# Performance work log

Measured on AMD Instinct MI355X. Metric: run time of the kernel, lower is better.

## Reference

```python
import jax, jax.numpy as jnp
import numpy as np

B, T, D, H = 2, 2048, 1024, 16
HD = D // H  # head_dim = 64


def setup_inputs() -> dict:
    key = jax.random.key(0)
    ks = jax.random.split(key, 6)
    x = jax.random.normal(ks[0], (B, T, D), dtype=jnp.float32)
    wq = jax.random.normal(ks[1], (D, D), dtype=jnp.float32) * (D ** -0.5)
    wk = jax.random.normal(ks[2], (D, D), dtype=jnp.float32) * (D ** -0.5)
    wv = jax.random.normal(ks[3], (D, D), dtype=jnp.float32) * (D ** -0.5)
    wo = jax.random.normal(ks[4], (D, D), dtype=jnp.float32) * (D ** -0.5)
    # RoPE tables: standard inverse-frequency angles, shape [T, head_dim]
    inv_freq = 1.0 / (10000.0 ** (jnp.arange(0, HD, 2, dtype=jnp.float32) / HD))
    ang = jnp.arange(T, dtype=jnp.float32)[:, None] * inv_freq[None, :]  # [T, HD/2]
    ang = jnp.concatenate([ang, ang], axis=-1)  # [T, HD]
    cos, sin = jnp.cos(ang), jnp.sin(ang)
    # causal mask [1,1,T,T]: True where attention is allowed
    mask = jnp.tril(jnp.ones((T, T), dtype=bool))[None, None]
    return {"x": x, "wq": wq, "wk": wk, "wv": wv, "wo": wo,
            "cos": cos, "sin": sin, "mask": mask}


def rotate_half(u):
    u1, u2 = jnp.split(u, 2, axis=-1)
    return jnp.concatenate([-u2, u1], axis=-1)


def reference(x, wq, wk, wv, wo, cos, sin, mask):
    b, t, c = x.shape
    # projections (nn.Linear: y = x @ W^T), reshape to [B, H, T, HD]
    def proj(w):
        return (x @ w.T).reshape(b, t, H, HD).transpose(0, 2, 1, 3)
    q, k, v = proj(wq), proj(wk), proj(wv)
    # inline RoPE: cos/sin broadcast [1,1,T,HD]
    co = cos[:t][None, None]
    si = sin[:t][None, None]
    q = q * co + rotate_half(q) * si
    k = k * co + rotate_half(k) * si
    # scaled dot-product attention with causal mask
    att = jnp.einsum("bhqd,bhkd->bhqk", q, k) * (HD ** -0.5)
    att = jnp.where(mask[:, :, :t, :t], att, -jnp.inf)
    att = jax.nn.softmax(att, axis=-1)
    out = jnp.einsum("bhqk,bhkd->bhqd", att, v)
    out = out.transpose(0, 2, 1, 3).reshape(b, t, c)
    return out @ wo.T
```

## Files before the change

### kernel.cpp

```cpp
#include <hip/hip_runtime.h>
#include <hip/hip_bf16.h>
#include <type_traits>

#define B_  2
#define T_  2048
#define D_  1024
#define H_  16
#define HD_ 64

typedef __attribute__((ext_vector_type(8))) short bf16x8;
typedef __attribute__((ext_vector_type(4))) float f32x4;

__device__ __forceinline__ unsigned short f2b(float x) {
  union { __hip_bfloat16 h; unsigned short u; } c;
  c.h = __float2bfloat16(x);
  return c.u;
}
__device__ __forceinline__ float b2f(unsigned short u) {
  union { unsigned short u; __hip_bfloat16 h; } c;
  c.u = u;
  return __bfloat162float(c.h);
}

__device__ __forceinline__ void ld_g2l_16(const unsigned short* g, unsigned short* l) {
  auto gp = (const __attribute__((address_space(1))) unsigned int*)g;
  auto lp = (__attribute__((address_space(3))) unsigned int*)l;
  __builtin_amdgcn_global_load_lds(gp, lp, 16, 0, 0);
}

__global__ void __launch_bounds__(256)
cast_all(const float* __restrict__ x, const float* __restrict__ wq,
         const float* __restrict__ wk, const float* __restrict__ wv,
         const float* __restrict__ wo, unsigned short* __restrict__ xb,
         unsigned short* __restrict__ wp) {
  int blk = blockIdx.x;
  const float* src;
  unsigned short* dst;
  size_t off;
  if (blk < 2048) {
    src = x; dst = xb; off = (size_t)blk * 2048;
  } else {
    int t = (blk - 2048) >> 9;
    int r = (blk - 2048) & 511;
    src = (t == 0) ? wq : (t == 1) ? wk : (t == 2) ? wv : wo;
    dst = wp + (size_t)t * 1048576;
    off = (size_t)r * 2048;
  }
  size_t i = off + threadIdx.x * 8;
  float4 a = *(const float4*)(src + i);
  float4 b = *(const float4*)(src + i + 4);
  unsigned short h[8] = {f2b(a.x), f2b(a.y), f2b(a.z), f2b(a.w),
                         f2b(b.x), f2b(b.y), f2b(b.z), f2b(b.w)};
  *(uint4*)(dst + i) = *(uint4*)h;
}

template <typename OutT, int MROWS>
__device__ __forceinline__ void gemm_core(const unsigned short* __restrict__ A,
                                          const unsigned short* __restrict__ Bw,
                                          OutT* __restrict__ C, int K, int Ldc,
                                          int rope_mode, const float* __restrict__ cosT,
                                          const float* __restrict__ sinT, int tok0) {
  constexpr int MT = MROWS / 32;
  constexpr int ASZ = MROWS * 32;
  __shared__ __align__(16) unsigned short shm[2 * ASZ + 2 * 128 * 32];
  const int tid = threadIdx.x;
  const int lane = tid & 63;
  const int w = tid >> 6;
  const int m16 = lane & 15;
  const int quad = lane >> 4;
  const int wm = w >> 1, wn = w & 1;
  const int rl = lane >> 2;
  const int cl = (lane & 3) * 8;

  auto a_sp = [&](int bs) { return &shm[bs * ASZ]; };
  auto b_sp = [&](int bs) { return &shm[2 * ASZ + bs * 4096]; };

  f32x4 acc[MT][4];
#pragma unroll
  for (int i = 0; i < MT; i++)
#pragma unroll
    for (int j = 0; j < 4; j++) acc[i][j] = (f32x4){0.f, 0.f, 0.f, 0.f};

  auto stage = [&](int it, int bs) {
    int k0 = it * 32;
#pragma unroll
    for (int t = 0; t < MROWS / 64; t++) {
      int seg = w * 16 + t * 64;
      ld_g2l_16(A + (size_t)(seg + rl) * K + k0 + cl, a_sp(bs) + seg * 32);
    }
#pragma unroll
    for (int j2 = 0; j2 < 2; j2++) {
      int seg = w * 32 + j2 * 16;
      ld_g2l_16(Bw + (size_t)(seg + rl) * K + k0 + cl, b_sp(bs) + seg * 32);
    }
  };

  const int nit = K / 32;
  stage(0, 0);
  __syncthreads();
  for (int it = 0; it < nit; it++) {
    int cur = it & 1;
    if (it + 1 < nit) stage(it + 1, cur ^ 1);
    bf16x8 af[MT], bfr[4];
#pragma unroll
    for (int mt = 0; mt < MT; mt++)
      af[mt] = *(const bf16x8*)(a_sp(cur) + (wm * (MT * 16) + mt * 16 + m16) * 32 + quad * 8);
#pragma unroll
    for (int nt = 0; nt < 4; nt++)
      bfr[nt] = *(const bf16x8*)(b_sp(cur) + (wn * 64 + nt * 16 + m16) * 32 + quad * 8);
#pragma unroll
    for (int mt = 0; mt < MT; mt++)
#pragma unroll
      for (int nt = 0; nt < 4; nt++)
        acc[mt][nt] = __builtin_amdgcn_mfma_f32_16x16x32_bf16(af[mt], bfr[nt], acc[mt][nt], 0, 0, 0);
    __syncthreads();
  }

  if (rope_mode == 3) {
    if constexpr (std::is_same_v<OutT, unsigned short> && MROWS == 128) {
#pragma unroll
      for (int p = 0; p < 2; p++) {
        if (wn == p) {
#pragma unroll
          for (int mt = 0; mt < MT; mt++)
#pragma unroll
            for (int nt = 0; nt < 4; nt++) {
              int r = nt * 16 + m16;
              int s = wm * 16 + mt * 4 + quad;
              unsigned short pk[4] = {f2b(acc[mt][nt][0]), f2b(acc[mt][nt][1]),
                                      f2b(acc[mt][nt][2]), f2b(acc[mt][nt][3])};
              *(uint2*)&shm[r * 136 + s * 4] = *(uint2*)pk;
            }
        }
        __syncthreads();
#pragma unroll
        for (int i = 0; i < 8; i++) {
          int li = i * 256 + tid;
          int r = li >> 5, s = li & 31;
          *(uint2*)(C + (size_t)(p * 64 + r) * T_ + s * 4) =
              *(const uint2*)&shm[r * 136 + s * 4];
        }
        __syncthreads();
      }
    }
    return;
  }

  if (rope_mode == 1 || rope_mode == 2) {
    float scale = (rope_mode == 2) ? 0.18033688011112042f : 1.f;
#pragma unroll
    for (int mt = 0; mt < MT; mt++)
#pragma unroll
      for (int reg = 0; reg < 4; reg++) {
        int t = (tok0 + wm * (MT * 16) + mt * 16 + quad * 4 + reg) & (T_ - 1);
#pragma unroll
        for (int nt = 0; nt < 2; nt++) {
          int d = nt * 16 + m16;
          float co = cosT[t * HD_ + d] * scale;
          float si = sinT[t * HD_ + d] * scale;
          float lo = acc[mt][nt][reg], hi = acc[mt][nt + 2][reg];
          acc[mt][nt][reg]     = lo * co - hi * si;
          acc[mt][nt + 2][reg] = hi * co + lo * si;
        }
      }
  }
#pragma unroll
  for (int mt = 0; mt < MT; mt++)
#pragma unroll
    for (int nt = 0; nt < 4; nt++)
#pragma unroll
      for (int reg = 0; reg < 4; reg++) {
        OutT* p = C + (size_t)(wm * (MT * 16) + mt * 16 + quad * 4 + reg) * Ldc + wn * 64 + nt * 16 + m16;
        if constexpr (std::is_same_v<OutT, float>) *p = acc[mt][nt][reg];
        else *p = f2b(acc[mt][nt][reg]);
      }
}

__global__ void __launch_bounds__(256)
gemm_qkv(const unsigned short* __restrict__ xb, const unsigned short* __restrict__ wp,
         unsigned short* __restrict__ qkv, const float* __restrict__ cosT,
         const float* __restrict__ sinT) {
  const int nb = blockIdx.x;
  const int bm = blockIdx.y * 128;
  const int mi = nb >> 3;
  const int bn = (nb & 7) * 128;
  if (mi == 2) {
    unsigned short* Cv = qkv + 2 * (4096ull * D_) +
                         (size_t)(bm >> 11) * (size_t)(H_ * HD_) * T_ +
                         (size_t)bn * T_ + (bm & (T_ - 1));
    gemm_core<unsigned short, 128>(xb + (size_t)bm * D_,
                                   wp + (size_t)(2 * 1024 + bn) * D_,
                                   Cv, D_, T_, 3, nullptr, nullptr, bm);
  } else {
    const int rope_mode = (mi == 0) ? 2 : 1;
    gemm_core<unsigned short, 128>(xb + (size_t)bm * D_,
                                   wp + (size_t)(mi * 1024 + bn) * D_,
                                   qkv + (size_t)mi * (4096ull * D_) + (size_t)bm * D_ + bn,
                                   D_, D_, rope_mode, cosT, sinT, bm);
  }
}

__global__ void __launch_bounds__(256)
gemm_out(const unsigned short* __restrict__ Ab, const unsigned short* __restrict__ wob,
         float* __restrict__ C) {
  const int bn = blockIdx.x * 128;
  const int bm = blockIdx.y * 64;
  gemm_core<float, 64>(Ab + (size_t)bm * D_, wob + (size_t)bn * D_,
                       C + (size_t)bm * D_ + bn, D_, D_, 0, nullptr, nullptr, 0);
}

__global__ void __launch_bounds__(256, 3)
attn_kernel(const unsigned short* __restrict__ Q, const unsigned short* __restrict__ K,
            const unsigned short* __restrict__ VT, unsigned short* __restrict__ O) {
  __shared__ __align__(16) unsigned short qp_s[64][72];
  __shared__ __align__(16) unsigned short k_s[2][64 * 64];
  __shared__ __align__(16) unsigned short vt_s[2][64 * 64];

  const int tid = threadIdx.x;
  const int lane = tid & 63;
  const int w = tid >> 6;
  const int m16 = lane & 15;
  const int quad = lane >> 4;
  const int swz = m16 & 7;
  const int pc0 = quad ^ swz;
  const int pc1 = pc0 ^ 4;

  const int x = blockIdx.x;
  const int qt = 31 - (x >> 5);
  const int bh = x & 31;
  const int b = bh >> 4, h = bh & 15;
  const int q0 = qt * 64;

  const unsigned short* Qb = Q + ((size_t)b * T_ + q0) * D_ + h * HD_;
  const unsigned short* Kb = K + (size_t)b * T_ * D_ + h * HD_;
  const unsigned short* VTb = VT + ((size_t)b * H_ + h) * HD_ * T_;

#pragma unroll
  for (int i = 0; i < 2; i++) {
    int idx = tid + i * 256;
    int r = idx >> 3, c = idx & 7;
    *(bf16x8*)&qp_s[r][c * 8] = *(const bf16x8*)(Qb + (size_t)r * D_ + c * 8);
  }

  auto stage_kv = [&](int kt, int bs) {
    int rs = lane >> 3;
    int cs = ((lane & 7) ^ rs) * 8;
    int gr = w * 16 + rs;
    ld_g2l_16(Kb + (size_t)(kt * 64 + gr) * D_ + cs,      &k_s[bs][(w * 16) * 64]);
    ld_g2l_16(Kb + (size_t)(kt * 64 + gr + 8) * D_ + cs,  &k_s[bs][(w * 16 + 8) * 64]);
    ld_g2l_16(VTb + (size_t)gr * T_ + kt * 64 + cs,       &vt_s[bs][(w * 16) * 64]);
    ld_g2l_16(VTb + (size_t)(gr + 8) * T_ + kt * 64 + cs, &vt_s[bs][(w * 16 + 8) * 64]);
  };

  f32x4 o_acc[4];
#pragma unroll
  for (int dt = 0; dt < 4; dt++) o_acc[dt] = (f32x4){0.f, 0.f, 0.f, 0.f};
  float m_i = -1e30f, l_i = 0.f;
  const int rg = q0 + w * 16 + m16;

  stage_kv(0, 0);
  __syncthreads();
  bf16x8 q_frag[2];
  q_frag[0] = *(const bf16x8*)&qp_s[w * 16 + m16][quad * 8];
  q_frag[1] = *(const bf16x8*)&qp_s[w * 16 + m16][32 + quad * 8];

  for (int t = 0; t <= qt; t++) {
    int cur = t & 1;
    if (t < qt) stage_kv(t + 1, cur ^ 1);

    const unsigned short* kc = &k_s[cur][0];
    const unsigned short* vc = &vt_s[cur][0];
    f32x4 sf[4];
    __builtin_amdgcn_s_setprio(1);
#pragma unroll
    for (int jt = 0; jt < 4; jt++) {
      bf16x8 a0 = *(const bf16x8*)&kc[(jt * 16 + m16) * 64 + pc0 * 8];
      bf16x8 a1 = *(const bf16x8*)&kc[(jt * 16 + m16) * 64 + pc1 * 8];
      f32x4 acc = (f32x4){0.f, 0.f, 0.f, 0.f};
      acc = __builtin_amdgcn_mfma_f32_16x16x32_bf16(a0, q_frag[0], acc, 0, 0, 0);
      acc = __builtin_amdgcn_mfma_f32_16x16x32_bf16(a1, q_frag[1], acc, 0, 0, 0);
      sf[jt] = acc;
    }
    __builtin_amdgcn_s_setprio(0);
    if (t == qt) {
#pragma unroll
      for (int jt = 0; jt < 4; jt++)
#pragma unroll
        for (int reg = 0; reg < 4; reg++) {
          int jg = t * 64 + jt * 16 + quad * 4 + reg;
          if (jg > rg) sf[jt][reg] = -1e30f;
        }
    }
    float mx = sf[0][0];
#pragma unroll
    for (int jt = 0; jt < 4; jt++)
#pragma unroll
      for (int reg = 0; reg < 4; reg++) mx = fmaxf(mx, sf[jt][reg]);
    mx = fmaxf(mx, __shfl_xor(mx, 16, 64));
    mx = fmaxf(mx, __shfl_xor(mx, 32, 64));
    if (!__all(mx <= m_i + 8.f)) {
      float mn = fmaxf(m_i, mx);
      float alpha = exp2f(m_i - mn);
      l_i *= alpha;
#pragma unroll
      for (int dt = 0; dt < 4; dt++)
#pragma unroll
        for (int reg = 0; reg < 4; reg++) o_acc[dt][reg] *= alpha;
      m_i = mn;
    }
    float lt = 0.f;
    float p[4][4];
#pragma unroll
    for (int jt = 0; jt < 4; jt++)
#pragma unroll
      for (int reg = 0; reg < 4; reg++) {
        p[jt][reg] = exp2f(sf[jt][reg] - m_i);
        lt += p[jt][reg];
      }
#pragma unroll
    for (int jt = 0; jt < 4; jt++) {
      unsigned short pk[4] = {f2b(p[jt][0]), f2b(p[jt][1]), f2b(p[jt][2]), f2b(p[jt][3])};
      *(uint2*)&qp_s[w * 16 + m16][jt * 16 + quad * 4] = *(uint2*)pk;
    }
    bf16x8 bp0 = *(const bf16x8*)&qp_s[w * 16 + m16][quad * 8];
    bf16x8 bp1 = *(const bf16x8*)&qp_s[w * 16 + m16][32 + quad * 8];
    __builtin_amdgcn_s_setprio(1);
#pragma unroll
    for (int dt = 0; dt < 4; dt++) {
      int rowd = dt * 16 + m16;
      bf16x8 a0 = *(const bf16x8*)&vc[rowd * 64 + pc0 * 8];
      bf16x8 a1 = *(const bf16x8*)&vc[rowd * 64 + pc1 * 8];
      o_acc[dt] = __builtin_amdgcn_mfma_f32_16x16x32_bf16(a0, bp0, o_acc[dt], 0, 0, 0);
      o_acc[dt] = __builtin_amdgcn_mfma_f32_16x16x32_bf16(a1, bp1, o_acc[dt], 0, 0, 0);
    }
    __builtin_amdgcn_s_setprio(0);
    lt += __shfl_xor(lt, 16, 64);
    lt += __shfl_xor(lt, 32, 64);
    l_i += lt;
    __syncthreads();
  }

  float inv = 1.f / l_i;
#pragma unroll
  for (int dt = 0; dt < 4; dt++) {
    unsigned short ok[4];
#pragma unroll
    for (int reg = 0; reg < 4; reg++) ok[reg] = f2b(o_acc[dt][reg] * inv);
    *(uint2*)&qp_s[w * 16 + m16][dt * 16 + quad * 4] = *(uint2*)ok;
  }
  __syncthreads();
  unsigned short* Ob = O + ((size_t)b * T_ + q0) * D_ + h * HD_;
#pragma unroll
  for (int i = 0; i < 2; i++) {
    int idx = tid + i * 256;
    int r = idx >> 3, c = idx & 7;
    *(bf16x8*)(Ob + (size_t)r * D_ + c * 8) = *(const bf16x8*)&qp_s[r][c * 8];
  }
}

extern "C" void kernel_launch(void* const* d_in, const int* in_sizes, int n_in,
                              void* d_out, int out_size, void* d_ws, size_t ws_size,
                              hipStream_t stream) {
  const float* x    = (const float*)d_in[0];
  const float* wq   = (const float*)d_in[1];
  const float* wk   = (const float*)d_in[2];
  const float* wv   = (const float*)d_in[3];
  const float* wo   = (const float*)d_in[4];
  const float* cosT = (const float*)d_in[5];
  const float* sinT = (const float*)d_in[6];
  float* out = (float*)d_out;

  const size_t NTOK = (size_t)B_ * T_;
  const size_t SZ   = NTOK * D_;
  unsigned short* xb   = (unsigned short*)d_ws;
  unsigned short* Wp   = xb + SZ;
  unsigned short* QKVh = Wp + 4 * 1048576;
  unsigned short* Ab   = QKVh + 3 * SZ;

  cast_all<<<4096, 256, 0, stream>>>(x, wq, wk, wv, wo, xb, Wp);
  gemm_qkv<<<dim3(24, 32), 256, 0, stream>>>(xb, Wp, QKVh, cosT, sinT);
  attn_kernel<<<1024, 256, 0, stream>>>(QKVh, QKVh + SZ, QKVh + 2 * SZ, Ab);
  gemm_out<<<dim3(8, 64), 256, 0, stream>>>(Ab, Wp + 3 * 1048576, out);
}
```

Measured before the change: 203.5 us.

## Fuse all four stages into one persistent cooperative kernel with grid syncs

Replaces the four separate launches (cast, QKV GEMM, attention, output GEMM) with a single cooperative kernel of 768 blocks that runs each stage in turn, separated by grid-wide barriers. The four launch gaps and tail idle time are meant to go away. Attention work is redistributed so blocks 0-255 take two q-tiles, paired as x and 1023-x, and the rest take one, to balance the causal workload. Shared memory is a single pool sized for the largest stage. Risks are the cost of grid.sync, occupancy limited to 3 blocks per CU, and the output GEMM using only 512 of the blocks. It falls back to the old four launches if the cooperative launch fails.

Result: slower. 651.3 us (+220.1%).

```diff
diff --git a/kernel.cpp b/kernel.cpp
--- a/kernel.cpp
+++ b/kernel.cpp
@@ -1,12 +1,16 @@
 #include <hip/hip_runtime.h>
 #include <hip/hip_bf16.h>
+#include <hip/hip_cooperative_groups.h>
 #include <type_traits>
+
+namespace cg = cooperative_groups;
 
 #define B_  2
 #define T_  2048
 #define D_  1024
 #define H_  16
 #define HD_ 64
+#define NB_ 768
 
 typedef __attribute__((ext_vector_type(8))) short bf16x8;
 typedef __attribute__((ext_vector_type(4))) float f32x4;
@@ -16,11 +20,6 @@
   c.h = __float2bfloat16(x);
   return c.u;
 }
-__device__ __forceinline__ float b2f(unsigned short u) {
-  union { unsigned short u; __hip_bfloat16 h; } c;
-  c.u = u;
-  return __bfloat162float(c.h);
-}
 
 __device__ __forceinline__ void ld_g2l_16(const unsigned short* g, unsigned short* l) {
   auto gp = (const __attribute__((address_space(1))) unsigned int*)g;
@@ -28,12 +27,11 @@
   __builtin_amdgcn_global_load_lds(gp, lp, 16, 0, 0);
 }
 
-__global__ void __launch_bounds__(256)
-cast_all(const float* __restrict__ x, const float* __restrict__ wq,
-         const float* __restrict__ wk, const float* __restrict__ wv,
-         const float* __restrict__ wo, unsigned short* __restrict__ xb,
-         unsigned short* __restrict__ wp) {
-  int blk = blockIdx.x;
+__device__ __forceinline__ void cast_job(int blk, const float* __restrict__ x,
+                                         const float* __restrict__ wq, const float* __restrict__ wk,
+                                         const float* __restrict__ wv, const float* __restrict__ wo,
+                                         unsigned short* __restrict__ xb,
+                                         unsigned short* __restrict__ wp) {
   const float* src;
   unsigned short* dst;
   size_t off;
@@ -55,14 +53,14 @@
 }
 
 template <typename OutT, int MROWS>
-__device__ __forceinline__ void gemm_core(const unsigned short* __restrict__ A,
+__device__ __forceinline__ void gemm_core(unsigned short* __restrict__ shm,
+                                          const unsigned short* __restrict__ A,
                                           const unsigned short* __restrict__ Bw,
                                           OutT* __restrict__ C, int K, int Ldc,
                                           int rope_mode, const float* __restrict__ cosT,
                                           const float* __restrict__ sinT, int tok0) {
   constexpr int MT = MROWS / 32;
   constexpr int ASZ = MROWS * 32;
-  __shared__ __align__(16) unsigned short shm[2 * ASZ + 2 * 128 * 32];
   const int tid = threadIdx.x;
   const int lane = tid & 63;
   const int w = tid >> 6;
@@ -72,9 +70,6 @@
   const int rl = lane >> 2;
   const int cl = (lane & 3) * 8;
 
-  auto a_sp = [&](int bs) { return &shm[bs * ASZ]; };
-  auto b_sp = [&](int bs) { return &shm[2 * ASZ + bs * 4096]; };
-
   f32x4 acc[MT][4];
 #pragma unroll
   for (int i = 0; i < MT; i++)
@@ -86,12 +81,12 @@
 #pragma unroll
     for (int t = 0; t < MROWS / 64; t++) {
       int seg = w * 16 + t * 64;
-      ld_g2l_16(A + (size_t)(seg + rl) * K + k0 + cl, a_sp(bs) + seg * 32);
+      ld_g2l_16(A + (size_t)(seg + rl) * K + k0 + cl, shm + bs * ASZ + seg * 32);
     }
 #pragma unroll
     for (int j2 = 0; j2 < 2; j2++) {
       int seg = w * 32 + j2 * 16;
-      ld_g2l_16(Bw + (size_t)(seg + rl) * K + k0 + cl, b_sp(bs) + seg * 32);
+      ld_g2l_16(Bw + (size_t)(seg + rl) * K + k0 + cl, shm + 2 * ASZ + bs * 4096 + seg * 32);
     }
   };
 
@@ -104,10 +99,10 @@
     bf16x8 af[MT], bfr[4];
 #pragma unroll
     for (int mt = 0; mt < MT; mt++)
-      af[mt] = *(const bf16x8*)(a_sp(cur) + (wm * (MT * 16) + mt * 16 + m16) * 32 + quad * 8);
+      af[mt] = *(const bf16x8*)(shm + cur * ASZ + (wm * (MT * 16) + mt * 16 + m16) * 32 + quad * 8);
 #pragma unroll
     for (int nt = 0; nt < 4; nt++)
-      bfr[nt] = *(const bf16x8*)(b_sp(cur) + (wn * 64 + nt * 16 + m16) * 32 + quad * 8);
+      bfr[nt] = *(const bf16x8*)(shm + 2 * ASZ + cur * 4096 + (wn * 64 + nt * 16 + m16) * 32 + quad * 8);
 #pragma unroll
     for (int mt = 0; mt < MT; mt++)
 #pragma unroll
@@ -176,45 +171,38 @@
       }
 }
 
-__global__ void __launch_bounds__(256)
-gemm_qkv(const unsigned short* __restrict__ xb, const unsigned short* __restrict__ wp,
-         unsigned short* __restrict__ qkv, const float* __restrict__ cosT,
-         const float* __restrict__ sinT) {
-  const int nb = blockIdx.x;
-  const int bm = blockIdx.y * 128;
+__device__ __forceinline__ void qkv_job(unsigned short* shm, int nb, int bm,
+                                        const unsigned short* __restrict__ xb,
+                                        const unsigned short* __restrict__ wp,
+                                        unsigned short* __restrict__ qkv,
+                                        const float* __restrict__ cosT,
+                                        const float* __restrict__ sinT) {
   const int mi = nb >> 3;
   const int bn = (nb & 7) * 128;
   if (mi == 2) {
     unsigned short* Cv = qkv + 2 * (4096ull * D_) +
                          (size_t)(bm >> 11) * (size_t)(H_ * HD_) * T_ +
                          (size_t)bn * T_ + (bm & (T_ - 1));
-    gemm_core<unsigned short, 128>(xb + (size_t)bm * D_,
+    gemm_core<unsigned short, 128>(shm, xb + (size_t)bm * D_,
                                    wp + (size_t)(2 * 1024 + bn) * D_,
                                    Cv, D_, T_, 3, nullptr, nullptr, bm);
   } else {
     const int rope_mode = (mi == 0) ? 2 : 1;
-    gemm_core<unsigned short, 128>(xb + (size_t)bm * D_,
+    gemm_core<unsigned short, 128>(shm, xb + (size_t)bm * D_,
                                    wp + (size_t)(mi * 1024 + bn) * D_,
                                    qkv + (size_t)mi * (4096ull * D_) + (size_t)bm * D_ + bn,
                                    D_, D_, rope_mode, cosT, sinT, bm);
   }
 }
 
-__global__ void __launch_bounds__(256)
-gemm_out(const unsigned short* __restrict__ Ab, const unsigned short* __restrict__ wob,
-         float* __restrict__ C) {
-  const int bn = blockIdx.x * 128;
-  const int bm = blockIdx.y * 64;
-  gemm_core<float, 64>(Ab + (size_t)bm * D_, wob + (size_t)bn * D_,
-                       C + (size_t)bm * D_ + bn, D_, D_, 0, nullptr, nullptr, 0);
-}
-
-__global__ void __launch_bounds__(256, 3)
-attn_kernel(const unsigned short* __restrict__ Q, const unsigned short* __restrict__ K,
-            const unsigned short* __restrict__ VT, unsigned short* __restrict__ O) {
-  __shared__ __align__(16) unsigned short qp_s[64][72];
-  __shared__ __align__(16) unsigned short k_s[2][64 * 64];
-  __shared__ __align__(16) unsigned short vt_s[2][64 * 64];
+__device__ __forceinline__ void attn_job(unsigned short* pool, int x,
+                                         const unsigned short* __restrict__ Q,
+                                         const unsigned short* __restrict__ K,
+                                         const unsigned short* __restrict__ VT,
+                                         unsigned short* __restrict__ O) {
+  unsigned short* qp = pool;
+  unsigned short* ks = pool + 4608;
+  unsigned short* vs = pool + 4608 + 8192;
 
   const int tid = threadIdx.x;
   const int lane = tid & 63;
@@ -225,7 +213,6 @@
   const int pc0 = quad ^ swz;
   const int pc1 = pc0 ^ 4;
 
-  const int x = blockIdx.x;
   const int qt = 31 - (x >> 5);
   const int bh = x & 31;
   const int b = bh >> 4, h = bh & 15;
@@ -239,17 +226,17 @@
   for (int i = 0; i < 2; i++) {
     int idx = tid + i * 256;
     int r = idx >> 3, c = idx & 7;
-    *(bf16x8*)&qp_s[r][c * 8] = *(const bf16x8*)(Qb + (size_t)r * D_ + c * 8);
+    *(bf16x8*)&qp[r * 72 + c * 8] = *(const bf16x8*)(Qb + (size_t)r * D_ + c * 8);
   }
 
   auto stage_kv = [&](int kt, int bs) {
     int rs = lane >> 3;
     int cs = ((lane & 7) ^ rs) * 8;
     int gr = w * 16 + rs;
-    ld_g2l_16(Kb + (size_t)(kt * 64 + gr) * D_ + cs,      &k_s[bs][(w * 16) * 64]);
-    ld_g2l_16(Kb + (size_t)(kt * 64 + gr + 8) * D_ + cs,  &k_s[bs][(w * 16 + 8) * 64]);
-    ld_g2l_16(VTb + (size_t)gr * T_ + kt * 64 + cs,       &vt_s[bs][(w * 16) * 64]);
-    ld_g2l_16(VTb + (size_t)(gr + 8) * T_ + kt * 64 + cs, &vt_s[bs][(w * 16 + 8) * 64]);
+    ld_g2l_16(Kb + (size_t)(kt * 64 + gr) * D_ + cs,      ks + bs * 4096 + (w * 16) * 64);
+    ld_g2l_16(Kb + (size_t)(kt * 64 + gr + 8) * D_ + cs,  ks + bs * 4096 + (w * 16 + 8) * 64);
+    ld_g2l_16(VTb + (size_t)gr * T_ + kt * 64 + cs,       vs + bs * 4096 + (w * 16) * 64);
+    ld_g2l_16(VTb + (size_t)(gr + 8) * T_ + kt * 64 + cs, vs + bs * 4096 + (w * 16 + 8) * 64);
   };
 
   f32x4 o_acc[4];
@@ -261,15 +248,15 @@
   stage_kv(0, 0);
   __syncthreads();
   bf16x8 q_frag[2];
-  q_frag[0] = *(const bf16x8*)&qp_s[w * 16 + m16][quad * 8];
-  q_frag[1] = *(const bf16x8*)&qp_s[w * 16 + m16][32 + quad * 8];
+  q_frag[0] = *(const bf16x8*)&qp[(w * 16 + m16) * 72 + quad * 8];
+  q_frag[1] = *(const bf16x8*)&qp[(w * 16 + m16) * 72 + 32 + quad * 8];
 
   for (int t = 0; t <= qt; t++) {
     int cur = t & 1;
     if (t < qt) stage_kv(t + 1, cur ^ 1);
 
-    const unsigned short* kc = &k_s[cur][0];
-    const unsigned short* vc = &vt_s[cur][0];
+    const unsigned short* kc = ks + cur * 4096;
+    const unsigned short* vc = vs + cur * 4096;
     f32x4 sf[4];
     __builtin_amdgcn_s_setprio(1);
 #pragma unroll
@@ -320,10 +307,10 @@
 #pragma unroll
     for (int jt = 0; jt < 4; jt++) {
       unsigned short pk[4] = {f2b(p[jt][0]), f2b(p[jt][1]), f2b(p[jt][2]), f2b(p[jt][3])};
-      *(uint2*)&qp_s[w * 16 + m16][jt * 16 + quad * 4] = *(uint2*)pk;
-    }
-    bf16x8 bp0 = *(const bf16x8*)&qp_s[w * 16 + m16][quad * 8];
-    bf16x8 bp1 = *(const bf16x8*)&qp_s[w * 16 + m16][32 + quad * 8];
+      *(uint2*)&qp[(w * 16 + m16) * 72 + jt * 16 + quad * 4] = *(uint2*)pk;
+    }
+    bf16x8 bp0 = *(const bf16x8*)&qp[(w * 16 + m16) * 72 + quad * 8];
+    bf16x8 bp1 = *(const bf16x8*)&qp[(w * 16 + m16) * 72 + 32 + quad * 8];
     __builtin_amdgcn_s_setprio(1);
 #pragma unroll
     for (int dt = 0; dt < 4; dt++) {
@@ -346,7 +333,7 @@
     unsigned short ok[4];
 #pragma unroll
     for (int reg = 0; reg < 4; reg++) ok[reg] = f2b(o_acc[dt][reg] * inv);
-    *(uint2*)&qp_s[w * 16 + m16][dt * 16 + quad * 4] = *(uint2*)ok;
+    *(uint2*)&qp[(w * 16 + m16) * 72 + dt * 16 + quad * 4] = *(uint2*)ok;
   }
   __syncthreads();
   unsigned short* Ob = O + ((size_t)b * T_ + q0) * D_ + h * HD_;
@@ -354,8 +341,81 @@
   for (int i = 0; i < 2; i++) {
     int idx = tid + i * 256;
     int r = idx >> 3, c = idx & 7;
-    *(bf16x8*)(Ob + (size_t)r * D_ + c * 8) = *(const bf16x8*)&qp_s[r][c * 8];
-  }
+    *(bf16x8*)(Ob + (size_t)r * D_ + c * 8) = *(const bf16x8*)&qp[r * 72 + c * 8];
+  }
+}
+
+__global__ void __launch_bounds__(256, 3)
+fused_all(const float* __restrict__ x, const float* __restrict__ wq,
+          const float* __restrict__ wk, const float* __restrict__ wv,
+          const float* __restrict__ wo, const float* __restrict__ cosT,
+          const float* __restrict__ sinT, unsigned short* __restrict__ xb,
+          unsigned short* __restrict__ wp, unsigned short* __restrict__ qkv,
+          unsigned short* __restrict__ Ab, float* __restrict__ out) {
+  __shared__ __align__(16) unsigned short pool[20992];
+  cg::grid_group grid = cg::this_grid();
+  const int bid = blockIdx.x;
+  const size_t SZ = 4096ull * D_;
+
+  for (int j = bid; j < 4096; j += NB_)
+    cast_job(j, x, wq, wk, wv, wo, xb, wp);
+  __threadfence();
+  grid.sync();
+
+  qkv_job(pool, bid % 24, (bid / 24) * 128, xb, wp, qkv, cosT, sinT);
+  __threadfence();
+  grid.sync();
+
+  if (bid < 256) {
+    attn_job(pool, bid, qkv, qkv + SZ, qkv + 2 * SZ, Ab);
+    __syncthreads();
+    attn_job(pool, 1023 - bid, qkv, qkv + SZ, qkv + 2 * SZ, Ab);
+  } else if (bid < 512) {
+    attn_job(pool, bid, qkv, qkv + SZ, qkv + 2 * SZ, Ab);
+  } else {
+    attn_job(pool, 1279 - bid, qkv, qkv + SZ, qkv + 2 * SZ, Ab);
+  }
+  __threadfence();
+  grid.sync();
+
+  if (bid < 512)
+    gemm_core<float, 64>(pool, Ab + (size_t)((bid >> 3) * 64) * D_,
+                         wp + 3 * 1048576 + (size_t)((bid & 7) * 128) * D_,
+                         out + (size_t)((bid >> 3) * 64) * D_ + (bid & 7) * 128,
+                         D_, D_, 0, nullptr, nullptr, 0);
+}
+
+__global__ void __launch_bounds__(256)
+cast_all(const float* __restrict__ x, const float* __restrict__ wq,
+         const float* __restrict__ wk, const float* __restrict__ wv,
+         const float* __restrict__ wo, unsigned short* __restrict__ xb,
+         unsigned short* __restrict__ wp) {
+  cast_job(blockIdx.x, x, wq, wk, wv, wo, xb, wp);
+}
+
+__global__ void __launch_bounds__(256)
+gemm_qkv(const unsigned short* __restrict__ xb, const unsigned short* __restrict__ wp,
+         unsigned short* __restrict__ qkv, const float* __restrict__ cosT,
+         const float* __restrict__ sinT) {
+  __shared__ __align__(16) unsigned short shm[16384];
+  qkv_job(shm, blockIdx.x, blockIdx.y * 128, xb, wp, qkv, cosT, sinT);
+}
+
+__global__ void __launch_bounds__(256)
+gemm_out(const unsigned short* __restrict__ Ab, const unsigned short* __restrict__ wob,
+         float* __restrict__ C) {
+  __shared__ __align__(16) unsigned short shm[12288];
+  const int bn = blockIdx.x * 128;
+  const int bm = blockIdx.y * 64;
+  gemm_core<float, 64>(shm, Ab + (size_t)bm * D_, wob + (size_t)bn * D_,
+                       C + (size_t)bm * D_ + bn, D_, D_, 0, nullptr, nullptr, 0);
+}
+
+__global__ void __launch_bounds__(256, 3)
+attn_kernel(const unsigned short* __restrict__ Q, const unsigned short* __restrict__ K,
+            const unsigned short* __restrict__ VT, unsigned short* __restrict__ O) {
+  __shared__ __align__(16) unsigned short pool[20992];
+  attn_job(pool, blockIdx.x, Q, K, VT, O);
 }
 
 extern "C" void kernel_launch(void* const* d_in, const int* in_sizes, int n_in,
@@ -377,8 +437,15 @@
   unsigned short* QKVh = Wp + 4 * 1048576;
   unsigned short* Ab   = QKVh + 3 * SZ;
 
-  cast_all<<<4096, 256, 0, stream>>>(x, wq, wk, wv, wo, xb, Wp);
-  gemm_qkv<<<dim3(24, 32), 256, 0, stream>>>(xb, Wp, QKVh, cosT, sinT);
-  attn_kernel<<<1024, 256, 0, stream>>>(QKVh, QKVh + SZ, QKVh + 2 * SZ, Ab);
-  gemm_out<<<dim3(8, 64), 256, 0, stream>>>(Ab, Wp + 3 * 1048576, out);
-}
+  void* args[] = {(void*)&x, (void*)&wq, (void*)&wk, (void*)&wv, (void*)&wo,
+                  (void*)&cosT, (void*)&sinT, (void*)&xb, (void*)&Wp,
+                  (void*)&QKVh, (void*)&Ab, (void*)&out};
+  hipError_t e = hipLaunchCooperativeKernel((const void*)fused_all, dim3(NB_),
+                                            dim3(256), args, 0, stream);
+  if (e != hipSuccess) {
+    cast_all<<<4096, 256, 0, stream>>>(x, wq, wk, wv, wo, xb, Wp);
+    gemm_qkv<<<dim3(24, 32), 256, 0, stream>>>(xb, Wp, QKVh, cosT, sinT);
+    attn_kernel<<<1024, 256, 0, stream>>>(QKVh, QKVh + SZ, QKVh + 2 * SZ, Ab);
+    gemm_out<<<dim3(8, 64), 256, 0, stream>>>(Ab, Wp + 3 * 1048576, out);
+  }
+}
```
